# Optimization experiments

Hardware: AMD Instinct MI355X
Metric: run time of the kernel (lower is better)

## Reference

```python
import jax, jax.numpy as jnp
import numpy as np

N, E = 50000, 800000
IN, HID, OUT = 128, 256, 128
BN_EPS = 1e-5


def setup_inputs() -> dict:
    key = jax.random.key(0)
    ks = jax.random.split(key, 12)
    x = jax.random.normal(ks[0], (N, IN), dtype=jnp.float32)
    edge_index = jax.random.randint(ks[1], (2, E), 0, N, dtype=jnp.int64)
    edge_weight = jax.random.uniform(ks[2], (E,), dtype=jnp.float32)
    # GCNConv weights (glorot-ish scale) and biases
    W0 = jax.random.normal(ks[3], (IN, HID), dtype=jnp.float32) * (1.0 / np.sqrt(IN))
    b0 = jnp.zeros((HID,), jnp.float32)
    W1 = jax.random.normal(ks[4], (HID, HID), dtype=jnp.float32) * (1.0 / np.sqrt(HID))
    b1 = jnp.zeros((HID,), jnp.float32)
    Wl = jax.random.normal(ks[5], (HID, OUT), dtype=jnp.float32) * (1.0 / np.sqrt(HID))
    bl = jnp.zeros((OUT,), jnp.float32)
    # BatchNorm affine params (eval mode: running_mean=0, running_var=1)
    g0 = 1.0 + 0.1 * jax.random.normal(ks[6], (HID,), dtype=jnp.float32)
    be0 = 0.1 * jax.random.normal(ks[7], (HID,), dtype=jnp.float32)
    g1 = 1.0 + 0.1 * jax.random.normal(ks[8], (HID,), dtype=jnp.float32)
    be1 = 0.1 * jax.random.normal(ks[9], (HID,), dtype=jnp.float32)
    return {"x": x, "edge_index": edge_index, "edge_weight": edge_weight,
            "W0": W0, "b0": b0, "W1": W1, "b1": b1, "Wl": Wl, "bl": bl,
            "g0": g0, "be0": be0, "g1": g1, "be1": be1}


def reference(x, edge_index, edge_weight, W0, b0, W1, b1, Wl, bl, g0, be0, g1, be1):
    n = x.shape[0]
    row, col = edge_index[0], edge_index[1]
    # add self-loops with weight 1 (GCNConv default)
    ar = jnp.arange(n)
    rowf = jnp.concatenate([row, ar])
    colf = jnp.concatenate([col, ar])
    wf = jnp.concatenate([edge_weight, jnp.ones((n,), x.dtype)])
    # symmetric normalization: D^{-1/2} A D^{-1/2}
    deg = jax.ops.segment_sum(wf, colf, num_segments=n)
    dinv = jnp.where(deg > 0, jax.lax.rsqrt(deg), 0.0)
    norm = dinv[rowf] * wf * dinv[colf]  # [E+N]

    def conv(h, W, b):
        h = h @ W                       # [n, d_out]
        msg = h[rowf] * norm[:, None]   # gather + scale per edge
        return jax.ops.segment_sum(msg, colf, num_segments=n) + b

    def bn_eval(h, g, b):
        # eval-mode BN with running_mean=0, running_var=1
        return h * (g / jnp.sqrt(1.0 + BN_EPS)) + b

    h = jax.nn.relu(bn_eval(conv(x, W0, b0), g0, be0))
    h = jax.nn.relu(bn_eval(conv(h, W1, b1), g1, be1))
    h = conv(h, Wl, bl)
    return jax.nn.log_softmax(h, axis=1)
```

## Files before the change

### kernel.cpp

```cpp
#include <hip/hip_runtime.h>
#include <cstddef>
#include <cstdint>


#define GCN_BN_EPS 1e-5f
#define NB_CHUNK 256

typedef short v8bf __attribute__((ext_vector_type(8)));
typedef float v4f __attribute__((ext_vector_type(4)));


__device__ __forceinline__ float4 unpack_bf4(uint2 u) {
  float4 r;
  r.x = __uint_as_float(u.x << 16);
  r.y = __uint_as_float(u.x & 0xffff0000u);
  r.z = __uint_as_float(u.y << 16);
  r.w = __uint_as_float(u.y & 0xffff0000u);
  return r;
}
__device__ __forceinline__ uint16_t f2bf(float f) {
  uint32_t u = __float_as_uint(f);
  return (uint16_t)((u + 0x7fffu + ((u >> 16) & 1u)) >> 16);
}
__device__ __forceinline__ uint2 pack_bf4(float4 v) {
  uint2 r;
  r.x = (uint32_t)f2bf(v.x) | ((uint32_t)f2bf(v.y) << 16);
  r.y = (uint32_t)f2bf(v.z) | ((uint32_t)f2bf(v.w) << 16);
  return r;
}
__device__ __forceinline__ float f16tof(unsigned int hi16) {
  return (float)__builtin_bit_cast(_Float16, (unsigned short)hi16);
}


__global__ __launch_bounds__(256) void build_hist_kernel(
    const int* __restrict__ ei, const float* __restrict__ ew,
    int* __restrict__ col_, uint2* __restrict__ pk,
    unsigned int* __restrict__ histw, float* __restrict__ degw, int E, int n) {
  extern __shared__ unsigned int h8[];
  __shared__ int s_flag;
  const int b = blockIdx.x;
  const int nw = (n + 3) >> 2;
  if (threadIdx.x == 0) {
    int nz = 0;
    for (int k = 1; k < 64; k += 2) nz |= ei[k];
    s_flag = (nz == 0) ? 1 : 0;
  }
  for (int i = threadIdx.x; i < nw; i += 256) h8[i] = 0u;
  __syncthreads();
  const int flag = s_flag;
  const int per = (E + NB_CHUNK - 1) / NB_CHUNK;
  const int e0 = b * per, e1 = min(e0 + per, E);
  for (int e = e0 + threadIdx.x; e < e1; e += 256) {
    int r, c;
    if (flag) { r = ei[2 * e]; c = ei[2 * (E + e)]; }
    else      { r = ei[e];     c = ei[E + e]; }
    float w = ew[e];
    col_[e] = c;
    pk[e] = make_uint2((unsigned)r, __float_as_uint(w));
    atomicAdd(&h8[c >> 2], 1u << ((c & 3) * 8));
    atomicAdd(&degw[c], w);
  }
  __syncthreads();
  for (int i = threadIdx.x; i < nw; i += 256)
    histw[(size_t)b * nw + i] = h8[i];
}

__global__ __launch_bounds__(256) void scan1_conv_kernel(
    const unsigned int* __restrict__ histw, unsigned int* __restrict__ cntw,
    int* __restrict__ bsum, int nw, int nB,
    const float* __restrict__ x, uint16_t* __restrict__ xb,
    const float* __restrict__ W0, uint16_t* __restrict__ W0t,
    const float* __restrict__ W1, uint16_t* __restrict__ W1t,
    const float* __restrict__ Wl, uint16_t* __restrict__ Wlt,
    const float* __restrict__ degw, float* __restrict__ dinv,
    int t0, int convTot) {
  if (blockIdx.x >= nB) {
    int i = (blockIdx.x - nB) * 256 + threadIdx.x;
    if (i >= convTot) return;
    if (i < t0) {
      float4 v = *(const float4*)&x[(size_t)i * 4];
      *(uint2*)&xb[(size_t)i * 4] = pack_bf4(v);
      return;
    }
    int j = i - t0;
    if (j < 128 * 256) { int nn = j >> 7, k = j & 127; W0t[j] = f2bf(W0[(size_t)k * 256 + nn]); return; }
    j -= 128 * 256;
    if (j < 256 * 256) { int nn = j >> 8, k = j & 255; W1t[j] = f2bf(W1[(size_t)k * 256 + nn]); return; }
    j -= 256 * 256;
    if (j < 256 * 128) { int nn = j >> 8, k = j & 255; Wlt[j] = f2bf(Wl[(size_t)k * 128 + nn]); return; }
    j -= 256 * 128;
    dinv[j] = rsqrtf(1.0f + degw[j]);
    return;
  }
  __shared__ int ws[4];
  const int j = blockIdx.x * 256 + threadIdx.x;
  unsigned int acc = 0;
  if (j < nw)
    for (int b = 0; b < NB_CHUNK; ++b) acc += histw[(size_t)b * nw + j];
  if (j < nw) cntw[j] = acc;
  int s = (int)((acc & 0xffu) + ((acc >> 8) & 0xffu) + ((acc >> 16) & 0xffu) + (acc >> 24));
  int x_ = s;
#pragma unroll
  for (int st = 1; st < 64; st <<= 1) x_ += __shfl_xor(x_, st, 64);
  if ((threadIdx.x & 63) == 0) ws[threadIdx.x >> 6] = x_;
  __syncthreads();
  if (threadIdx.x == 0) bsum[blockIdx.x] = ws[0] + ws[1] + ws[2] + ws[3];
}

__global__ __launch_bounds__(256) void scan3_base_kernel(
    const unsigned int* __restrict__ cntw, const int* __restrict__ bsum,
    int* __restrict__ off, unsigned int* __restrict__ histw,
    int nw, int nB, int n, int E) {
  __shared__ int wsum[4], woff[4];
  __shared__ int s_gbase;
  const int tid = threadIdx.x, lane = tid & 63, wv = tid >> 6;
  const int j = blockIdx.x * 256 + tid;
  unsigned int cw = (j < nw) ? cntw[j] : 0u;
  const int c0 = (int)(cw & 0xffu), c1 = (int)((cw >> 8) & 0xffu);
  const int c2 = (int)((cw >> 16) & 0xffu), c3 = (int)(cw >> 24);
  int s = c0 + c1 + c2 + c3;
  int x = s;
#pragma unroll
  for (int st = 1; st < 64; st <<= 1) { int t = __shfl_up(x, st, 64); if (lane >= st) x += t; }
  if (lane == 63) wsum[wv] = x;
  __syncthreads();
  if (tid == 0) { int r = 0; for (int k = 0; k < 4; ++k) { woff[k] = r; r += wsum[k]; } }
  if (wv == 0) {
    int v2 = (lane < nB) ? bsum[lane] : 0;
    int y = v2;
#pragma unroll
    for (int st = 1; st < 64; st <<= 1) { int t = __shfl_up(y, st, 64); if (lane >= st) y += t; }
    if (lane == blockIdx.x) s_gbase = y - v2;
  }
  __syncthreads();
  if (j < nw) {
    int excl = x - s + woff[wv] + s_gbase;
    uint4 o4;
    o4.x = excl; o4.y = excl + c0; o4.z = excl + c0 + c1; o4.w = excl + c0 + c1 + c2;
    *(uint4*)&off[4 * j] = o4;
    unsigned int run = 0;
    for (int b = 0; b < NB_CHUNK; ++b) {
      size_t idx = (size_t)b * nw + j;
      unsigned int w = histw[idx];
      histw[idx] = run;
      run += w;
    }
  }
  if (blockIdx.x == 0 && tid == 0) off[n] = E;
}

__global__ __launch_bounds__(256) void fill_kernel(
    const int* __restrict__ col_, const uint2* __restrict__ pk,
    const int* __restrict__ off, const unsigned int* __restrict__ histw,
    const float* __restrict__ dinv, unsigned int* __restrict__ csr4,
    int E, int n) {
  extern __shared__ unsigned int c8[];
  const int b = blockIdx.x;
  const int nw = (n + 3) >> 2;
  for (int i = threadIdx.x; i < nw; i += 256) c8[i] = 0u;
  __syncthreads();
  const int per = (E + NB_CHUNK - 1) / NB_CHUNK;
  const int e0 = b * per, e1 = min(e0 + per, E);
  const unsigned int* brel = histw + (size_t)b * nw;
  for (int e = e0 + threadIdx.x; e < e1; e += 256) {
    int c = col_[e];
    const int sh = (c & 3) * 8;
    unsigned old = atomicAdd(&c8[c >> 2], 1u << sh);
    int rel = (int)((old >> sh) & 0xffu) + (int)((brel[c >> 2] >> sh) & 0xffu);
    uint2 v = pk[e];
    float nv = dinv[(int)v.x] * __uint_as_float(v.y);
    unsigned short hb = __builtin_bit_cast(unsigned short, (_Float16)nv);
    csr4[off[c] + rel] = (v.x & 0xffffu) | ((unsigned int)hb << 16);
  }
}


template <int EPI>
__global__ __launch_bounds__(256) void agg256_kernel(
    const uint16_t* __restrict__ hin, uint16_t* __restrict__ hout,
    const int* __restrict__ off, const unsigned int* __restrict__ csr4,
    const float* __restrict__ dinv,
    const float* __restrict__ bias, const float* __restrict__ g,
    const float* __restrict__ be, int n) {
  const int lane = threadIdx.x & 63;
  const int c = blockIdx.x * 4 + (threadIdx.x >> 6);
  if (c >= n) return;
  const int f = lane * 4;
  const int e0 = off[c], e1 = off[c + 1];
  const float di = dinv[c];
  float4 self = unpack_bf4(*(const uint2*)&hin[(size_t)c * 256 + f]);
  float4 acc = make_float4(self.x * di, self.y * di, self.z * di, self.w * di);

  for (int base = e0; base < e1; base += 64) {
    int idx = base + lane;
    unsigned int ev = (idx < e1) ? __builtin_nontemporal_load(&csr4[idx]) : 0u;
    const int m = min(64, e1 - base);
    const int nG = (m + 3) >> 2;
    for (int gI = 0; gI < nG; ++gI) {
      int e_ = gI * 4;
      unsigned int ea = __shfl(ev, e_, 64);
      unsigned int eb = __shfl(ev, e_ + 1, 64);
      unsigned int ec = __shfl(ev, e_ + 2, 64);
      unsigned int ed = __shfl(ev, e_ + 3, 64);
      float v0 = f16tof(ea >> 16), v1 = f16tof(eb >> 16);
      float v2 = f16tof(ec >> 16), v3 = f16tof(ed >> 16);
      float4 h0 = unpack_bf4(*(const uint2*)&hin[(size_t)(ea & 0xffffu) * 256 + f]);
      float4 h1 = unpack_bf4(*(const uint2*)&hin[(size_t)(eb & 0xffffu) * 256 + f]);
      float4 h2 = unpack_bf4(*(const uint2*)&hin[(size_t)(ec & 0xffffu) * 256 + f]);
      float4 h3 = unpack_bf4(*(const uint2*)&hin[(size_t)(ed & 0xffffu) * 256 + f]);
      acc.x += v0 * h0.x + v1 * h1.x + v2 * h2.x + v3 * h3.x;
      acc.y += v0 * h0.y + v1 * h1.y + v2 * h2.y + v3 * h3.y;
      acc.z += v0 * h0.z + v1 * h1.z + v2 * h2.z + v3 * h3.z;
      acc.w += v0 * h0.w + v1 * h1.w + v2 * h2.w + v3 * h3.w;
    }
  }

  acc.x *= di; acc.y *= di; acc.z *= di; acc.w *= di;
  if (EPI == 1) {
    const float bns = rsqrtf(1.0f + GCN_BN_EPS);
    float4 bi = *(const float4*)&bias[f];
    float4 gi = *(const float4*)&g[f];
    float4 bei = *(const float4*)&be[f];
    acc.x = fmaxf((acc.x + bi.x) * gi.x * bns + bei.x, 0.0f);
    acc.y = fmaxf((acc.y + bi.y) * gi.y * bns + bei.y, 0.0f);
    acc.z = fmaxf((acc.z + bi.z) * gi.z * bns + bei.z, 0.0f);
    acc.w = fmaxf((acc.w + bi.w) * gi.w * bns + bei.w, 0.0f);
  }
  *(uint2*)&hout[(size_t)c * 256 + f] = pack_bf4(acc);
}

template <int EPI>
__global__ __launch_bounds__(256) void agg128_kernel(
    const uint16_t* __restrict__ hin, void* __restrict__ hout_,
    const int* __restrict__ off, const unsigned int* __restrict__ csr4,
    const float* __restrict__ dinv, const float* __restrict__ bias, int n) {
  const int lane = threadIdx.x & 63;
  const int sub = lane & 31;
  const int hbase = lane & 32;
  const int c = blockIdx.x * 8 + (threadIdx.x >> 6) * 2 + (lane >> 5);
  const bool active = (c < n);
  const int f = sub * 4;

  int e0 = 0, e1 = 0;
  float di = 0.0f;
  float4 acc = make_float4(0.f, 0.f, 0.f, 0.f);
  if (active) {
    e0 = off[c]; e1 = off[c + 1];
    di = dinv[c];
    float4 self = unpack_bf4(*(const uint2*)&hin[(size_t)c * 128 + f]);
    acc = make_float4(self.x * di, self.y * di, self.z * di, self.w * di);
  }
  int nch = (e1 - e0 + 31) >> 5;
  nch = max(nch, __shfl(nch, lane ^ 32));

  for (int ch = 0; ch < nch; ++ch) {
    int idx = e0 + ch * 32 + sub;
    unsigned int ev = 0u;
    if (active && idx < e1) ev = __builtin_nontemporal_load(&csr4[idx]);
    int m = e1 - (e0 + ch * 32);
    m = m < 0 ? 0 : (m > 32 ? 32 : m);
    int mMax = max(m, __shfl(m, lane ^ 32));
    const int nG = (mMax + 3) >> 2;
    for (int gI = 0; gI < nG; ++gI) {
      int e_ = hbase + gI * 4;
      unsigned int ea = __shfl(ev, e_, 64);
      unsigned int eb = __shfl(ev, e_ + 1, 64);
      unsigned int ec = __shfl(ev, e_ + 2, 64);
      unsigned int ed = __shfl(ev, e_ + 3, 64);
      int s0 = (int)(ea & 0xffffu); float v0 = f16tof(ea >> 16);
      int s1 = (int)(eb & 0xffffu); float v1 = f16tof(eb >> 16);
      int sB = (int)(ec & 0xffffu); float v2 = f16tof(ec >> 16);
      int s3 = (int)(ed & 0xffffu); float v3 = f16tof(ed >> 16);
      float4 h0 = unpack_bf4(*(const uint2*)&hin[(size_t)s0 * 128 + f]);
      float4 h1 = unpack_bf4(*(const uint2*)&hin[(size_t)s1 * 128 + f]);
      float4 h2 = unpack_bf4(*(const uint2*)&hin[(size_t)sB * 128 + f]);
      float4 h3 = unpack_bf4(*(const uint2*)&hin[(size_t)s3 * 128 + f]);
      acc.x += v0 * h0.x + v1 * h1.x + v2 * h2.x + v3 * h3.x;
      acc.y += v0 * h0.y + v1 * h1.y + v2 * h2.y + v3 * h3.y;
      acc.z += v0 * h0.z + v1 * h1.z + v2 * h2.z + v3 * h3.z;
      acc.w += v0 * h0.w + v1 * h1.w + v2 * h2.w + v3 * h3.w;
    }
  }

  acc.x *= di; acc.y *= di; acc.z *= di; acc.w *= di;
  if (EPI == 0) {
    uint16_t* hout = (uint16_t*)hout_;
    if (active) *(uint2*)&hout[(size_t)c * 128 + f] = pack_bf4(acc);
  } else {
    float* hout = (float*)hout_;
    float4 bi = active ? *(const float4*)&bias[f] : make_float4(0.f, 0.f, 0.f, 0.f);
    float tx = acc.x + bi.x, ty = acc.y + bi.y, tz = acc.z + bi.z, tw = acc.w + bi.w;
    float mx = fmaxf(fmaxf(tx, ty), fmaxf(tz, tw));
#pragma unroll
    for (int s = 1; s < 32; s <<= 1) mx = fmaxf(mx, __shfl_xor(mx, s, 64));
    float ex = expf(tx - mx) + expf(ty - mx) + expf(tz - mx) + expf(tw - mx);
#pragma unroll
    for (int s = 1; s < 32; s <<= 1) ex += __shfl_xor(ex, s, 64);
    float lse = logf(ex) + mx;
    if (active) {
      float4 res = make_float4(tx - lse, ty - lse, tz - lse, tw - lse);
      *(float4*)&hout[(size_t)c * 128 + f] = res;
    }
  }
}

template <int K, int NC, int EPI>
__global__ __launch_bounds__(256) void mfma_gemm_kernel(
    const uint16_t* __restrict__ A, const uint16_t* __restrict__ WT,
    uint16_t* __restrict__ Cb, int M, int tpb,
    const float* __restrict__ bias, const float* __restrict__ g,
    const float* __restrict__ be) {
  constexpr int CW = NC / 4;
  constexpr int NT = CW / 16;
  constexpr int KS = K / 32;
  const int lane = threadIdx.x & 63;
  const int wave = threadIdx.x >> 6;
  const int quad = lane >> 4;
  const int l16 = lane & 15;
  const int col0 = wave * CW;

  const int tiles = (M + 15) >> 4;
  int t0 = blockIdx.x * tpb;
  if (t0 >= tiles) return;
  int t1 = min(t0 + tpb, tiles);

  v8bf b[KS][NT];
#pragma unroll
  for (int ks = 0; ks < KS; ++ks)
#pragma unroll
    for (int nt = 0; nt < NT; ++nt)
      b[ks][nt] = *(const v8bf*)(WT + (size_t)(col0 + nt * 16 + l16) * K +
                                 ks * 32 + quad * 8);

  float sc[NT], o1[NT], o2[NT];
  if (EPI == 1) {
    const float bns = rsqrtf(1.0f + GCN_BN_EPS);
#pragma unroll
    for (int nt = 0; nt < NT; ++nt) {
      int col = col0 + nt * 16 + l16;
      sc[nt] = g[col] * bns; o1[nt] = bias[col]; o2[nt] = be[col];
    }
  }

  v8bf a[KS], an[KS];
  {
    int arow = min(t0 * 16 + l16, M - 1);
    const uint16_t* Ap = A + (size_t)arow * K + quad * 8;
#pragma unroll
    for (int ks = 0; ks < KS; ++ks) a[ks] = *(const v8bf*)(Ap + ks * 32);
  }
  for (int t = t0; t < t1; ++t) {
    if (t + 1 < t1) {
      int arow = min((t + 1) * 16 + l16, M - 1);
      const uint16_t* Ap = A + (size_t)arow * K + quad * 8;
#pragma unroll
      for (int ks = 0; ks < KS; ++ks) an[ks] = *(const v8bf*)(Ap + ks * 32);
    }
    v4f acc[NT];
#pragma unroll
    for (int nt = 0; nt < NT; ++nt) acc[nt] = (v4f){0.f, 0.f, 0.f, 0.f};
#pragma unroll
    for (int ks = 0; ks < KS; ++ks)
#pragma unroll
      for (int nt = 0; nt < NT; ++nt)
        acc[nt] = __builtin_amdgcn_mfma_f32_16x16x32_bf16(a[ks], b[ks][nt],
                                                          acc[nt], 0, 0, 0);
    const int row0 = t * 16 + quad * 4;
#pragma unroll
    for (int nt = 0; nt < NT; ++nt) {
      const int col = col0 + nt * 16 + l16;
#pragma unroll
      for (int r = 0; r < 4; ++r) {
        int row = row0 + r;
        if (row < M) {
          float v = acc[nt][r];
          if (EPI == 1) v = fmaxf((v + o1[nt]) * sc[nt] + o2[nt], 0.0f);
          Cb[(size_t)row * NC + col] = f2bf(v);
        }
      }
    }
#pragma unroll
    for (int ks = 0; ks < KS; ++ks) a[ks] = an[ks];
  }
}


static inline char* carve(char*& p, size_t bytes) {
  char* r = p;
  p += (bytes + 255) & ~(size_t)255;
  return r;
}

extern "C" void kernel_launch(void* const* d_in, const int* in_sizes, int n_in,
                              void* d_out, int out_size, void* d_ws, size_t ws_size,
                              hipStream_t stream) {
  const int N = in_sizes[0] / 128;
  const int E = in_sizes[2];

  const float* x  = (const float*)d_in[0];
  const int*   ei = (const int*)d_in[1];
  const float* ew = (const float*)d_in[2];
  const float* W0 = (const float*)d_in[3];
  const float* b0 = (const float*)d_in[4];
  const float* W1 = (const float*)d_in[5];
  const float* b1 = (const float*)d_in[6];
  const float* Wl = (const float*)d_in[7];
  const float* bl = (const float*)d_in[8];
  const float* g0 = (const float*)d_in[9];
  const float* be0 = (const float*)d_in[10];
  const float* g1 = (const float*)d_in[11];
  const float* be1 = (const float*)d_in[12];
  float* out = (float*)d_out;

  const int nw = (N + 3) / 4;

  char* p = (char*)d_ws;
  float*        dinv  = (float*)carve(p, (size_t)N * 4);
  float*        degw  = (float*)carve(p, (size_t)N * 4);
  unsigned int* cntw  = (unsigned int*)carve(p, (size_t)nw * 4);
  int*          off   = (int*)carve(p, (size_t)(N + 1) * 4);
  int*          bsum  = (int*)carve(p, 1024 * 4);
  int*          col_  = (int*)carve(p, (size_t)E * 4);
  uint2*        pk    = (uint2*)carve(p, (size_t)E * 8);
  unsigned int* csr4  = (unsigned int*)carve(p, (size_t)E * 4);
  unsigned int* histw = (unsigned int*)carve(p, (size_t)NB_CHUNK * nw * 4);
  uint16_t*     xb16  = (uint16_t*)carve(p, (size_t)N * 128 * 2);
  uint16_t*     bufR  = (uint16_t*)carve(p, (size_t)N * 128 * 2);
  uint16_t*     bufP  = (uint16_t*)carve(p, (size_t)N * 256 * 2);
  uint16_t*     bufQ  = (uint16_t*)carve(p, (size_t)N * 256 * 2);
  uint16_t*     W0t   = (uint16_t*)carve(p, (size_t)128 * 256 * 2);
  uint16_t*     W1t   = (uint16_t*)carve(p, (size_t)256 * 256 * 2);
  uint16_t*     Wlt   = (uint16_t*)carve(p, (size_t)256 * 128 * 2);

  const int TB = 256;
  const int gW4 = (N + 3) / 4;
  const int gW8 = (N + 7) / 8;
  const int tiles = (N + 15) / 16;
  const int TPB = 8;
  const int gG = (tiles + TPB - 1) / TPB;
  const size_t ldsU8 = (size_t)nw * 4;
  const int nB = (nw + 255) / 256;
  const int convT0 = N * 32;
  const int convTot = convT0 + 128 * 256 + 256 * 256 + 256 * 128 + N;
  const int convB = (convTot + TB - 1) / TB;

  hipMemsetAsync(degw, 0, (size_t)N * 4, stream);
  build_hist_kernel<<<NB_CHUNK, TB, ldsU8, stream>>>(ei, ew, col_, pk, histw,
                                                     degw, E, N);
  scan1_conv_kernel<<<nB + convB, TB, 0, stream>>>(histw, cntw, bsum, nw, nB,
                                                   x, xb16, W0, W0t, W1, W1t,
                                                   Wl, Wlt, degw, dinv,
                                                   convT0, convTot);
  scan3_base_kernel<<<nB, TB, 0, stream>>>(cntw, bsum, off, histw, nw, nB, N, E);
  fill_kernel<<<NB_CHUNK, TB, ldsU8, stream>>>(col_, pk, off, histw, dinv,
                                               csr4, E, N);

  agg128_kernel<0><<<gW8, 256, 0, stream>>>(xb16, bufR, off, csr4, dinv,
                                            nullptr, N);
  mfma_gemm_kernel<128, 256, 1><<<gG, 256, 0, stream>>>(bufR, W0t, bufP, N, TPB,
                                                        b0, g0, be0);
  mfma_gemm_kernel<256, 256, 0><<<gG, 256, 0, stream>>>(bufP, W1t, bufQ, N, TPB,
                                                        nullptr, nullptr, nullptr);
  agg256_kernel<1><<<gW4, 256, 0, stream>>>(bufQ, bufP, off, csr4, dinv,
                                            b1, g1, be1, N);
  mfma_gemm_kernel<256, 128, 0><<<gG, 256, 0, stream>>>(bufP, Wlt, bufR, N, TPB,
                                                        nullptr, nullptr, nullptr);
  agg128_kernel<2><<<gW8, 256, 0, stream>>>(bufR, out, off, csr4, dinv, bl, N);
}
```

Baseline: 385.6 us.

## Compute degree from CSR, pack edges as fp16, and scalarize agg256 loop

Drops the global float atomicAdd degree accumulation and its memset. The degree is instead computed per node from the filled CSR in a new kernel, and a separate pass rescales the CSR weights by dinv. Edges are now packed into 32-bit words (16-bit row, fp16 weight) at build time, which halves that buffer. The 256-wide aggregation is rewritten to read CSR entries with wave-uniform scalar loads and 8-way unrolled gathers instead of shuffles, and the GEMM tiles-per-block changes from 8 to 7. The change adds two kernel launches and one extra pass over the CSR, and the raw edge weight is now rounded to fp16 before the degree sum.

```diff
diff --git a/kernel.cpp b/kernel.cpp
--- a/kernel.cpp
+++ b/kernel.cpp
@@ -18,6 +18,8 @@
   r.w = __uint_as_float(u.y & 0xffff0000u);
   return r;
 }
+__device__ __forceinline__ float bflo(unsigned u) { return __uint_as_float(u << 16); }
+__device__ __forceinline__ float bfhi(unsigned u) { return __uint_as_float(u & 0xffff0000u); }
 __device__ __forceinline__ uint16_t f2bf(float f) {
   uint32_t u = __float_as_uint(f);
   return (uint16_t)((u + 0x7fffu + ((u >> 16) & 1u)) >> 16);
@@ -31,12 +33,19 @@
 __device__ __forceinline__ float f16tof(unsigned int hi16) {
   return (float)__builtin_bit_cast(_Float16, (unsigned short)hi16);
 }
+__device__ __forceinline__ unsigned ftof16b(float f) {
+  return (unsigned)__builtin_bit_cast(unsigned short, (_Float16)f);
+}
+__device__ __forceinline__ void fma_row4(float4& acc, float nv, uint2 u) {
+  acc.x += nv * bflo(u.x); acc.y += nv * bfhi(u.x);
+  acc.z += nv * bflo(u.y); acc.w += nv * bfhi(u.y);
+}
 
 
 __global__ __launch_bounds__(256) void build_hist_kernel(
     const int* __restrict__ ei, const float* __restrict__ ew,
-    int* __restrict__ col_, uint2* __restrict__ pk,
-    unsigned int* __restrict__ histw, float* __restrict__ degw, int E, int n) {
+    int* __restrict__ col_, unsigned int* __restrict__ pk4,
+    unsigned int* __restrict__ histw, int E, int n) {
   extern __shared__ unsigned int h8[];
   __shared__ int s_flag;
   const int b = blockIdx.x;
@@ -55,11 +64,9 @@
     int r, c;
     if (flag) { r = ei[2 * e]; c = ei[2 * (E + e)]; }
     else      { r = ei[e];     c = ei[E + e]; }
-    float w = ew[e];
     col_[e] = c;
-    pk[e] = make_uint2((unsigned)r, __float_as_uint(w));
+    pk4[e] = ((unsigned)r & 0xffffu) | (ftof16b(ew[e]) << 16);
     atomicAdd(&h8[c >> 2], 1u << ((c & 3) * 8));
-    atomicAdd(&degw[c], w);
   }
   __syncthreads();
   for (int i = threadIdx.x; i < nw; i += 256)
@@ -73,7 +80,6 @@
     const float* __restrict__ W0, uint16_t* __restrict__ W0t,
     const float* __restrict__ W1, uint16_t* __restrict__ W1t,
     const float* __restrict__ Wl, uint16_t* __restrict__ Wlt,
-    const float* __restrict__ degw, float* __restrict__ dinv,
     int t0, int convTot) {
   if (blockIdx.x >= nB) {
     int i = (blockIdx.x - nB) * 256 + threadIdx.x;
@@ -88,9 +94,7 @@
     j -= 128 * 256;
     if (j < 256 * 256) { int nn = j >> 8, k = j & 255; W1t[j] = f2bf(W1[(size_t)k * 256 + nn]); return; }
     j -= 256 * 256;
-    if (j < 256 * 128) { int nn = j >> 8, k = j & 255; Wlt[j] = f2bf(Wl[(size_t)k * 128 + nn]); return; }
-    j -= 256 * 128;
-    dinv[j] = rsqrtf(1.0f + degw[j]);
+    if (j < 256 * 128) { int nn = j >> 8, k = j & 255; Wlt[j] = f2bf(Wl[(size_t)k * 128 + nn]); }
     return;
   }
   __shared__ int ws[4];
@@ -151,10 +155,9 @@
 }
 
 __global__ __launch_bounds__(256) void fill_kernel(
-    const int* __restrict__ col_, const uint2* __restrict__ pk,
+    const int* __restrict__ col_, const unsigned int* __restrict__ pk4,
     const int* __restrict__ off, const unsigned int* __restrict__ histw,
-    const float* __restrict__ dinv, unsigned int* __restrict__ csr4,
-    int E, int n) {
+    unsigned int* __restrict__ csr4, int E, int n) {
   extern __shared__ unsigned int c8[];
   const int b = blockIdx.x;
   const int nw = (n + 3) >> 2;
@@ -168,52 +171,73 @@
     const int sh = (c & 3) * 8;
     unsigned old = atomicAdd(&c8[c >> 2], 1u << sh);
     int rel = (int)((old >> sh) & 0xffu) + (int)((brel[c >> 2] >> sh) & 0xffu);
-    uint2 v = pk[e];
-    float nv = dinv[(int)v.x] * __uint_as_float(v.y);
-    unsigned short hb = __builtin_bit_cast(unsigned short, (_Float16)nv);
-    csr4[off[c] + rel] = (v.x & 0xffffu) | ((unsigned int)hb << 16);
-  }
+    csr4[off[c] + rel] = pk4[e];
+  }
+}
+
+__global__ void degdinv_kernel(const int* __restrict__ off,
+                               const unsigned int* __restrict__ csr4,
+                               float* __restrict__ dinv, int n) {
+  int i = blockIdx.x * blockDim.x + threadIdx.x;
+  if (i >= n) return;
+  float s = 1.0f;
+  int p1 = off[i + 1];
+  for (int p = off[i]; p < p1; ++p) s += f16tof(csr4[p] >> 16);
+  dinv[i] = rsqrtf(s);
+}
+
+__global__ __launch_bounds__(256) void csr4conv_kernel(
+    const float* __restrict__ dinv, unsigned int* __restrict__ csr4, int E) {
+  int e = blockIdx.x * 256 + threadIdx.x;
+  if (e >= E) return;
+  unsigned v = csr4[e];
+  float nv = dinv[v & 0xffffu] * f16tof(v >> 16);
+  csr4[e] = (v & 0xffffu) | (ftof16b(nv) << 16);
 }
 
 
 template <int EPI>
-__global__ __launch_bounds__(256) void agg256_kernel(
+__global__ __launch_bounds__(256) void agg256s_kernel(
     const uint16_t* __restrict__ hin, uint16_t* __restrict__ hout,
     const int* __restrict__ off, const unsigned int* __restrict__ csr4,
     const float* __restrict__ dinv,
     const float* __restrict__ bias, const float* __restrict__ g,
     const float* __restrict__ be, int n) {
   const int lane = threadIdx.x & 63;
-  const int c = blockIdx.x * 4 + (threadIdx.x >> 6);
+  const int c = __builtin_amdgcn_readfirstlane(blockIdx.x * 4 + (threadIdx.x >> 6));
   if (c >= n) return;
   const int f = lane * 4;
   const int e0 = off[c], e1 = off[c + 1];
   const float di = dinv[c];
-  float4 self = unpack_bf4(*(const uint2*)&hin[(size_t)c * 256 + f]);
-  float4 acc = make_float4(self.x * di, self.y * di, self.z * di, self.w * di);
-
-  for (int base = e0; base < e1; base += 64) {
-    int idx = base + lane;
-    unsigned int ev = (idx < e1) ? __builtin_nontemporal_load(&csr4[idx]) : 0u;
-    const int m = min(64, e1 - base);
-    const int nG = (m + 3) >> 2;
-    for (int gI = 0; gI < nG; ++gI) {
-      int e_ = gI * 4;
-      unsigned int ea = __shfl(ev, e_, 64);
-      unsigned int eb = __shfl(ev, e_ + 1, 64);
-      unsigned int ec = __shfl(ev, e_ + 2, 64);
-      unsigned int ed = __shfl(ev, e_ + 3, 64);
-      float v0 = f16tof(ea >> 16), v1 = f16tof(eb >> 16);
-      float v2 = f16tof(ec >> 16), v3 = f16tof(ed >> 16);
-      float4 h0 = unpack_bf4(*(const uint2*)&hin[(size_t)(ea & 0xffffu) * 256 + f]);
-      float4 h1 = unpack_bf4(*(const uint2*)&hin[(size_t)(eb & 0xffffu) * 256 + f]);
-      float4 h2 = unpack_bf4(*(const uint2*)&hin[(size_t)(ec & 0xffffu) * 256 + f]);
-      float4 h3 = unpack_bf4(*(const uint2*)&hin[(size_t)(ed & 0xffffu) * 256 + f]);
-      acc.x += v0 * h0.x + v1 * h1.x + v2 * h2.x + v3 * h3.x;
-      acc.y += v0 * h0.y + v1 * h1.y + v2 * h2.y + v3 * h3.y;
-      acc.z += v0 * h0.z + v1 * h1.z + v2 * h2.z + v3 * h3.z;
-      acc.w += v0 * h0.w + v1 * h1.w + v2 * h2.w + v3 * h3.w;
-    }
+  const uint16_t* __restrict__ hrow = hin + (size_t)c * 256;
+  float4 acc = unpack_bf4(*(const uint2*)&hrow[f]);
+  acc.x *= di; acc.y *= di; acc.z *= di; acc.w *= di;
+
+  int e = e0;
+  for (; e + 8 <= e1; e += 8) {
+    unsigned v0 = csr4[e + 0], v1 = csr4[e + 1], v2 = csr4[e + 2], v3 = csr4[e + 3];
+    unsigned v4 = csr4[e + 4], v5 = csr4[e + 5], v6 = csr4[e + 6], v7 = csr4[e + 7];
+    uint2 h0 = *(const uint2*)&hin[(size_t)(v0 & 0xffffu) * 256 + f];
+    uint2 h1 = *(const uint2*)&hin[(size_t)(v1 & 0xffffu) * 256 + f];
+    uint2 h2 = *(const uint2*)&hin[(size_t)(v2 & 0xffffu) * 256 + f];
+    uint2 h3 = *(const uint2*)&hin[(size_t)(v3 & 0xffffu) * 256 + f];
+    uint2 h4 = *(const uint2*)&hin[(size_t)(v4 & 0xffffu) * 256 + f];
+    uint2 h5 = *(const uint2*)&hin[(size_t)(v5 & 0xffffu) * 256 + f];
+    uint2 h6 = *(const uint2*)&hin[(size_t)(v6 & 0xffffu) * 256 + f];
+    uint2 h7 = *(const uint2*)&hin[(size_t)(v7 & 0xffffu) * 256 + f];
+    fma_row4(acc, f16tof(v0 >> 16), h0);
+    fma_row4(acc, f16tof(v1 >> 16), h1);
+    fma_row4(acc, f16tof(v2 >> 16), h2);
+    fma_row4(acc, f16tof(v3 >> 16), h3);
+    fma_row4(acc, f16tof(v4 >> 16), h4);
+    fma_row4(acc, f16tof(v5 >> 16), h5);
+    fma_row4(acc, f16tof(v6 >> 16), h6);
+    fma_row4(acc, f16tof(v7 >> 16), h7);
+  }
+  for (; e < e1; ++e) {
+    unsigned v = csr4[e];
+    uint2 h = *(const uint2*)&hin[(size_t)(v & 0xffffu) * 256 + f];
+    fma_row4(acc, f16tof(v >> 16), h);
   }
 
   acc.x *= di; acc.y *= di; acc.z *= di; acc.w *= di;
@@ -417,12 +441,11 @@
 
   char* p = (char*)d_ws;
   float*        dinv  = (float*)carve(p, (size_t)N * 4);
-  float*        degw  = (float*)carve(p, (size_t)N * 4);
   unsigned int* cntw  = (unsigned int*)carve(p, (size_t)nw * 4);
   int*          off   = (int*)carve(p, (size_t)(N + 1) * 4);
   int*          bsum  = (int*)carve(p, 1024 * 4);
   int*          col_  = (int*)carve(p, (size_t)E * 4);
-  uint2*        pk    = (uint2*)carve(p, (size_t)E * 8);
+  unsigned int* pk4   = (unsigned int*)carve(p, (size_t)E * 4);
   unsigned int* csr4  = (unsigned int*)carve(p, (size_t)E * 4);
   unsigned int* histw = (unsigned int*)carve(p, (size_t)NB_CHUNK * nw * 4);
   uint16_t*     xb16  = (uint16_t*)carve(p, (size_t)N * 128 * 2);
@@ -434,27 +457,27 @@
   uint16_t*     Wlt   = (uint16_t*)carve(p, (size_t)256 * 128 * 2);
 
   const int TB = 256;
+  const int gN = (N + TB - 1) / TB;
   const int gW4 = (N + 3) / 4;
   const int gW8 = (N + 7) / 8;
+  const int gE = (E + TB - 1) / TB;
   const int tiles = (N + 15) / 16;
-  const int TPB = 8;
+  const int TPB = 7;
   const int gG = (tiles + TPB - 1) / TPB;
   const size_t ldsU8 = (size_t)nw * 4;
   const int nB = (nw + 255) / 256;
   const int convT0 = N * 32;
-  const int convTot = convT0 + 128 * 256 + 256 * 256 + 256 * 128 + N;
+  const int convTot = convT0 + 128 * 256 + 256 * 256 + 256 * 128;
   const int convB = (convTot + TB - 1) / TB;
 
-  hipMemsetAsync(degw, 0, (size_t)N * 4, stream);
-  build_hist_kernel<<<NB_CHUNK, TB, ldsU8, stream>>>(ei, ew, col_, pk, histw,
-                                                     degw, E, N);
+  build_hist_kernel<<<NB_CHUNK, TB, ldsU8, stream>>>(ei, ew, col_, pk4, histw, E, N);
   scan1_conv_kernel<<<nB + convB, TB, 0, stream>>>(histw, cntw, bsum, nw, nB,
                                                    x, xb16, W0, W0t, W1, W1t,
-                                                   Wl, Wlt, degw, dinv,
-                                                   convT0, convTot);
+                                                   Wl, Wlt, convT0, convTot);
   scan3_base_kernel<<<nB, TB, 0, stream>>>(cntw, bsum, off, histw, nw, nB, N, E);
-  fill_kernel<<<NB_CHUNK, TB, ldsU8, stream>>>(col_, pk, off, histw, dinv,
-                                               csr4, E, N);
+  fill_kernel<<<NB_CHUNK, TB, ldsU8, stream>>>(col_, pk4, off, histw, csr4, E, N);
+  degdinv_kernel<<<gN, TB, 0, stream>>>(off, csr4, dinv, N);
+  csr4conv_kernel<<<gE, TB, 0, stream>>>(dinv, csr4, E);
 
   agg128_kernel<0><<<gW8, 256, 0, stream>>>(xb16, bufR, off, csr4, dinv,
                                             nullptr, N);
@@ -462,8 +485,8 @@
                                                         b0, g0, be0);
   mfma_gemm_kernel<256, 256, 0><<<gG, 256, 0, stream>>>(bufP, W1t, bufQ, N, TPB,
                                                         nullptr, nullptr, nullptr);
-  agg256_kernel<1><<<gW4, 256, 0, stream>>>(bufQ, bufP, off, csr4, dinv,
-                                            b1, g1, be1, N);
+  agg256s_kernel<1><<<gW4, 256, 0, stream>>>(bufQ, bufP, off, csr4, dinv,
+                                             b1, g1, be1, N);
   mfma_gemm_kernel<256, 128, 0><<<gG, 256, 0, stream>>>(bufP, Wlt, bufR, N, TPB,
                                                         nullptr, nullptr, nullptr);
   agg128_kernel<2><<<gW8, 256, 0, stream>>>(bufR, out, off, csr4, dinv, bl, N);
```

Result: faster. 347.8 us (-9.8%).
